# Kernel optimization log

Measured on AMD Instinct MI355X. Metric: run time of the kernel, lower is better.

The kernel has to match this reference:

```python
import jax, jax.numpy as jnp
import numpy as np

N_HEADS = 16
NEG = -1e9  # matches torch masked_fill value


def setup_inputs() -> dict:
    key = jax.random.key(0)
    ks = jax.random.split(key, 8)
    B, S, E = 4, 1024, 1024
    x = jax.random.normal(ks[0], (B, S, E), dtype=jnp.float32)
    event_lengths = jax.random.randint(ks[1], (B,), 1, S + 1)
    scale = 1.0 / np.sqrt(E)
    Wq = jax.random.normal(ks[2], (E, E), dtype=jnp.float32) * scale
    bq = jnp.zeros((E,), dtype=jnp.float32)
    Wk = jax.random.normal(ks[3], (E, E), dtype=jnp.float32) * scale
    bk = jnp.zeros((E,), dtype=jnp.float32)
    Wv = jax.random.normal(ks[4], (E, E), dtype=jnp.float32) * scale
    bv = jnp.zeros((E,), dtype=jnp.float32)
    return {"x": x, "Wq": Wq, "bq": bq, "Wk": Wk, "bk": bk,
            "Wv": Wv, "bv": bv, "event_lengths": event_lengths}


def reference(x, Wq, bq, Wk, bk, Wv, bv, event_lengths):
    B, S, E = x.shape
    H = N_HEADS
    D = E // H
    # fused projections, then split heads: [B,S,E] -> [B,H,S,D]
    def split(t):
        return t.reshape(B, S, H, D).transpose(0, 2, 1, 3)
    q = split(x @ Wq + bq)
    k = split(x @ Wk + bk)
    v = split(x @ Wv + bv)
    scores = jnp.einsum('bhsd,bhtd->bhst', q, k) / jnp.sqrt(jnp.float32(D))
    # rectangular length mask: valid iff row < len AND col < len
    idx = jnp.arange(S)
    valid = idx[None, :] < event_lengths[:, None]           # [B,S]
    mask = valid[:, :, None] & valid[:, None, :]            # [B,S,S]
    scores = jnp.where(mask[:, None, :, :], scores, NEG)
    attn = jax.nn.softmax(scores, axis=-1)
    out = jnp.einsum('bhst,bhtd->bhsd', attn, v)            # [B,H,S,D]
    # concat heads (== torch.cat over head outputs); NOTE: summarize proj is
    # dead code in the original (its result is overwritten), dropout is eval-identity
    return out.transpose(0, 2, 1, 3).reshape(B, S, E)
```

## Files before the change

kernel.cpp:

```cpp
#include <hip/hip_runtime.h>
#include <stdint.h>


using u16     = unsigned short;
using half8   = __attribute__((ext_vector_type(8))) _Float16;
using floatx4 = __attribute__((ext_vector_type(4))) float;

#define MFMA16(a, b, c) __builtin_amdgcn_mfma_f32_16x16x32_f16(a, b, c, 0, 0, 0)

__device__ __forceinline__ u16 f2h(float f) {
  _Float16 h = (_Float16)f; u16 u; __builtin_memcpy(&u, &h, 2); return u;
}

__device__ __forceinline__ void async_cp16(void* lds, const void* g) {
  __builtin_amdgcn_global_load_lds(
      (__attribute__((address_space(1))) uint32_t*)(uintptr_t)g,
      (__attribute__((address_space(3))) uint32_t*)(uint32_t)(uintptr_t)lds,
      16, 0, 0);
}

__global__ void k_prep(const float* __restrict__ x, u16* __restrict__ xh,
                       const float* __restrict__ w0, const float* __restrict__ w1,
                       const float* __restrict__ w2,
                       u16* __restrict__ o0, u16* __restrict__ o1,
                       u16* __restrict__ o2, float* __restrict__ vsum) {
  __shared__ float t[32][33];
  const int bx = blockIdx.x;
  if (bx < 4096) {
    int i = (bx * 256 + threadIdx.x) * 4;
    float4 v = *(const float4*)(x + i);
    ushort4 hv;
    hv.x = f2h(v.x);
    hv.y = f2h(v.y);
    hv.z = f2h(v.z);
    hv.w = f2h(v.w);
    *(ushort4*)(xh + i) = hv;
    if (bx == 0) {
      float4 z = {0.f, 0.f, 0.f, 0.f};
#pragma unroll
      for (int e = 0; e < 4; e++) ((float4*)vsum)[threadIdx.x * 4 + e] = z;
    }
    return;
  }
  const int id = bx - 4096;
  const int z = id >> 10, rem = id & 1023;
  const float* W = z == 0 ? w0 : (z == 1 ? w1 : w2);
  u16* oh = z == 0 ? o0 : (z == 1 ? o1 : o2);
  const int kb = (rem & 31) * 32, nb = (rem >> 5) * 32;
  const int tx = threadIdx.x & 31, ty = threadIdx.x >> 5;
  for (int r = ty; r < 32; r += 8) t[r][tx] = W[(kb + r) * 1024 + nb + tx];
  __syncthreads();
  for (int r = ty; r < 32; r += 8)
    oh[(nb + r) * 1024 + kb + tx] = f2h(t[tx][r]);
}

__launch_bounds__(256, 4)
__global__ void k_proj(const u16* __restrict__ xh,
                       const u16* __restrict__ wqT, const u16* __restrict__ wkT,
                       const u16* __restrict__ wvT,
                       const float* __restrict__ bq, const float* __restrict__ bk,
                       const float* __restrict__ bv,
                       const int* __restrict__ elen,
                       u16* __restrict__ qh, u16* __restrict__ kh,
                       u16* __restrict__ vth, float* __restrict__ vsum) {
  __shared__ u16 Sm[17408];
  const int z = blockIdx.z;
  const int m0 = blockIdx.x * 128, n0 = blockIdx.y * 128;
  if (z != 2 && (m0 & 1023) >= elen[m0 >> 10]) return;

  const u16* wT = z == 0 ? wqT : (z == 1 ? wkT : wvT);
  const float* bias = z == 0 ? bq : (z == 1 ? bk : bv);
  u16* oh = z == 0 ? qh : (z == 1 ? kh : vth);
  const float oscale = (z == 0) ? 0.18033688011112042f : 1.0f;

  const int tid = threadIdx.x, l = tid & 63, w = tid >> 6;
  const int quad = l >> 4, col = l & 15;
  const int wm = (w & 1) * 64, wn = (w >> 1) * 64;

  const int row0 = tid >> 3, ch = tid & 7;
  const int sc8 = (ch ^ (row0 & 7)) * 8;
  int gofs[4], lofs[4];
#pragma unroll
  for (int p = 0; p < 4; p++) {
    gofs[p] = (row0 + 32 * p) * 1024 + sc8;
    lofs[p] = (tid + p * 256) * 8;
  }

  const u16* Ag = xh + m0 * 1024;
  const u16* Bg = wT + n0 * 1024;

  int ar[2][4], br[2][4];
#pragma unroll
  for (int ks = 0; ks < 2; ks++) {
#pragma unroll
    for (int i = 0; i < 4; i++) {
      int r = wm + i * 16 + col;
      ar[ks][i] = r * 64 + (((ks * 4 + quad) ^ (r & 7)) * 8);
    }
#pragma unroll
    for (int j = 0; j < 4; j++) {
      int r = wn + j * 16 + col;
      br[ks][j] = r * 64 + (((ks * 4 + quad) ^ (r & 7)) * 8);
    }
  }

  floatx4 zero4 = {0.f, 0.f, 0.f, 0.f};
  floatx4 acc[4][4];
#pragma unroll
  for (int i = 0; i < 4; i++)
#pragma unroll
    for (int j = 0; j < 4; j++) acc[i][j] = zero4;

  for (int k0 = 0; k0 < 1024; k0 += 64) {
    __syncthreads();
#pragma unroll
    for (int p = 0; p < 4; p++) async_cp16(Sm + lofs[p], Ag + gofs[p] + k0);
#pragma unroll
    for (int p = 0; p < 4; p++)
      async_cp16(Sm + 8192 + lofs[p], Bg + gofs[p] + k0);
    __syncthreads();

#pragma unroll
    for (int ks = 0; ks < 2; ks++) {
      half8 fa[4], fb[4];
#pragma unroll
      for (int i = 0; i < 4; i++) fa[i] = *(const half8*)(Sm + ar[ks][i]);
#pragma unroll
      for (int j = 0; j < 4; j++)
        fb[j] = *(const half8*)(Sm + 8192 + br[ks][j]);
#pragma unroll
      for (int i = 0; i < 4; i++)
#pragma unroll
        for (int j = 0; j < 4; j++) acc[i][j] = MFMA16(fa[i], fb[j], acc[i][j]);
    }
  }

  const int bidx = m0 >> 10;
  const int sbase = m0 & 1023;
  __syncthreads();

#pragma unroll
  for (int j = 0; j < 4; j++) {
    int nloc = wn + j * 16 + col;
    float bb = bias[n0 + nloc];
#pragma unroll
    for (int i = 0; i < 4; i++)
#pragma unroll
      for (int r = 0; r < 4; r++) {
        int mloc = wm + i * 16 + quad * 4 + r;
        Sm[mloc * 136 + nloc] = f2h((acc[i][j][r] + bb) * oscale);
      }
  }
  __syncthreads();

  if (z != 2) {
#pragma unroll
    for (int k = 0; k < 8; k++) {
      int c = tid + k * 256;
      int mloc = c >> 4, n = (c & 15) * 8;
      int hh = (n0 + n) >> 6, d = (n0 + n) & 63;
      half8 vv = *(const half8*)(Sm + mloc * 136 + n);
      *(half8*)(oh + ((bidx * 16 + hh) * 1024 + sbase + mloc) * 64 + d) = vv;
    }
  } else {
#pragma unroll
    for (int k = 0; k < 8; k++) {
      int c = tid + k * 256;
      int nloc = c & 127, s0 = (c >> 7) * 8;
      int hh = (n0 + nloc) >> 6, d = (n0 + nloc) & 63;
      u16 tmp[8];
#pragma unroll
      for (int e = 0; e < 8; e++) tmp[e] = Sm[(s0 + e) * 136 + nloc];
      *(half8*)(vth + ((bidx * 16 + hh) * 64 + d) * 1024 + sbase + s0) =
          *(half8*)tmp;
    }
#pragma unroll
    for (int j = 0; j < 4; j++) {
      int nloc = wn + j * 16 + col;
      float bb = bias[n0 + nloc];
      float part = 16.0f * bb;
#pragma unroll
      for (int i = 0; i < 4; i++)
#pragma unroll
        for (int r = 0; r < 4; r++) part += acc[i][j][r];
      part += __shfl_xor(part, 16, 64);
      part += __shfl_xor(part, 32, 64);
      if (quad == 0) {
        int hh = (n0 + nloc) >> 6, d = (n0 + nloc) & 63;
        unsafeAtomicAdd(vsum + (bidx * 16 + hh) * 64 + d, part);
      }
    }
  }
}

template <int NC>
__device__ __forceinline__ void stageN(u16* lds, const u16* g, int row_stride,
                                       int tid) {
#pragma unroll
  for (int p = 0; p < NC; p++) {
    int slot = (p * 512 + tid) * 8;
    int row = slot >> 6;
    int gp = (slot >> 3) & 7;
    int gl = gp ^ (row & 7);
    async_cp16(lds + slot, g + row * row_stride + gl * 8);
  }
}

__launch_bounds__(512)
__global__ void k_attn(const u16* __restrict__ qh_g,
                       const u16* __restrict__ kh_g,
                       const u16* __restrict__ vth_g,
                       const float* __restrict__ vsum, const int* __restrict__ elen,
                       float* __restrict__ out) {
  __shared__ u16 QP[8192];
  __shared__ u16 Bufs[2][8192];
  const int tid = threadIdx.x, l = tid & 63, w = tid >> 6;
  const int quad = l >> 4, col = l & 15;
  const int tb = w & 3;
  const int qh2 = w >> 2;
  const int id = blockIdx.x;
  const int b = (id + (id >> 8)) & 3;
  const int h = (id >> 2) & 15;
  const int bh = b * 16 + h;
  const int q0 = ((id >> 6) & 7) * 128;
  const int len = elen[b];

  if (q0 >= len) {
    float val = vsum[bh * 64 + l] * (1.0f / 1024.0f);
    float* op = out + (b * 1024 + q0) * 1024 + h * 64 + l;
    for (int r = w; r < 128; r += 8) op[r * 1024] = val;
    return;
  }

  const u16* kh_b  = kh_g + bh * 65536;
  const u16* vth_b = vth_g + bh * 65536;

  stageN<2>(QP, qh_g + (bh * 1024 + q0) * 64, 64, tid);
  stageN<1>(Bufs[0], kh_b, 64, tid);
  stageN<1>(Bufs[0] + 4096, vth_b, 1024, tid);
  __syncthreads();

  half8 qf[4][2];
#pragma unroll
  for (int jj = 0; jj < 4; jj++) {
    int qrow = (qh2 * 4 + jj) * 16 + col;
#pragma unroll
    for (int ks = 0; ks < 2; ks++)
      qf[jj][ks] = *(const half8*)(QP + qrow * 64 +
                                   (((ks * 4 + quad) ^ (qrow & 7)) * 8));
  }
  __syncthreads();

  int ko[2];
#pragma unroll
  for (int ks = 0; ks < 2; ks++) {
    int r = tb * 16 + col;
    ko[ks] = r * 64 + (((ks * 4 + quad) ^ (r & 7)) * 8);
  }
  int po[2];
#pragma unroll
  for (int ks = 0; ks < 2; ks++) {
    int r = w * 16 + col;
    po[ks] = r * 64 + (((ks * 4 + quad) ^ (r & 7)) * 8);
  }
  int kvo[2][4];
#pragma unroll
  for (int ks = 0; ks < 2; ks++)
#pragma unroll
    for (int j = 0; j < 4; j++) {
      int n = j * 16 + col;
      kvo[ks][j] = n * 64 + (((ks * 4 + quad) ^ (n & 7)) * 8);
    }
  int p_wr[4];
  {
    int chv = tb * 2 + (quad >> 1);
#pragma unroll
    for (int jj = 0; jj < 4; jj++) {
      int row = (qh2 * 4 + jj) * 16 + col;
      p_wr[jj] = row * 64 + ((chv ^ (row & 7)) * 8) + (quad & 1) * 4;
    }
  }

  floatx4 zero4 = {0.f, 0.f, 0.f, 0.f};
  floatx4 O[4];
  float lp[4];
#pragma unroll
  for (int j = 0; j < 4; j++) O[j] = zero4;
#pragma unroll
  for (int jj = 0; jj < 4; jj++) lp[jj] = 0.f;

  const int ntt = (len + 63) >> 6;
  for (int tt = 0; tt < ntt; ++tt) {
    const int t0 = tt * 64;
    u16* cur = Bufs[tt & 1];
    if (tt + 1 < ntt) {
      u16* nxt = Bufs[(tt + 1) & 1];
      const int t1 = t0 + 64;
      stageN<1>(nxt, kh_b + t1 * 64, 64, tid);
      stageN<1>(nxt + 4096, vth_b + t1, 1024, tid);
    }

    floatx4 sc[4];
#pragma unroll
    for (int jj = 0; jj < 4; jj++) sc[jj] = zero4;
#pragma unroll
    for (int ks = 0; ks < 2; ks++) {
      half8 kf = *(const half8*)(cur + ko[ks]);
#pragma unroll
      for (int jj = 0; jj < 4; jj++) sc[jj] = MFMA16(kf, qf[jj][ks], sc[jj]);
    }

    if (t0 + 64 > len) {
#pragma unroll
      for (int r = 0; r < 4; r++) {
        bool inv = (t0 + tb * 16 + quad * 4 + r) >= len;
#pragma unroll
        for (int jj = 0; jj < 4; jj++)
          if (inv) sc[jj][r] = -3e38f;
      }
    }

#pragma unroll
    for (int jj = 0; jj < 4; jj++) {
      float e0 = __builtin_exp2f(sc[jj][0]);
      float e1 = __builtin_exp2f(sc[jj][1]);
      float e2 = __builtin_exp2f(sc[jj][2]);
      float e3 = __builtin_exp2f(sc[jj][3]);
      lp[jj] += (e0 + e1) + (e2 + e3);
      uint2 pk;
      pk.x = (uint32_t)f2h(e0) | ((uint32_t)f2h(e1) << 16);
      pk.y = (uint32_t)f2h(e2) | ((uint32_t)f2h(e3) << 16);
      *(uint2*)(QP + p_wr[jj]) = pk;
    }

    asm volatile("s_waitcnt lgkmcnt(0)" ::: "memory");
    __builtin_amdgcn_s_barrier();
    __builtin_amdgcn_sched_barrier(0);

#pragma unroll
    for (int ks = 0; ks < 2; ks++) {
      half8 pa = *(const half8*)(QP + po[ks]);
#pragma unroll
      for (int j = 0; j < 4; j++) {
        half8 vb = *(const half8*)(cur + 4096 + kvo[ks][j]);
        O[j] = MFMA16(pa, vb, O[j]);
      }
    }

    __syncthreads();
  }

  float* lred = (float*)Bufs;
#pragma unroll
  for (int jj = 0; jj < 4; jj++) {
    float v = lp[jj];
    v += __shfl_xor(v, 16, 64);
    v += __shfl_xor(v, 32, 64);
    lp[jj] = v;
  }
  if (quad == 0) {
#pragma unroll
    for (int jj = 0; jj < 4; jj++)
      lred[tb * 128 + (qh2 * 4 + jj) * 16 + col] = lp[jj];
  }
  __syncthreads();

#pragma unroll
  for (int r = 0; r < 4; r++) {
    int qloc = w * 16 + quad * 4 + r;
    int s = q0 + qloc;
    float lr = (lred[qloc] + lred[128 + qloc]) +
               (lred[256 + qloc] + lred[384 + qloc]);
    float invl = 1.0f / lr;
    bool valid = (s < len);
#pragma unroll
    for (int j = 0; j < 4; j++) {
      int d = j * 16 + col;
      float val = valid ? O[j][r] * invl : vsum[bh * 64 + d] * (1.0f / 1024.0f);
      out[(b * 1024 + s) * 1024 + h * 64 + d] = val;
    }
  }
}

extern "C" void kernel_launch(void* const* d_in, const int* in_sizes, int n_in,
                              void* d_out, int out_size, void* d_ws, size_t ws_size,
                              hipStream_t stream) {
  (void)in_sizes; (void)n_in; (void)out_size; (void)ws_size;
  const float* x  = (const float*)d_in[0];
  const float* Wq = (const float*)d_in[1];
  const float* bq = (const float*)d_in[2];
  const float* Wk = (const float*)d_in[3];
  const float* bk = (const float*)d_in[4];
  const float* Wv = (const float*)d_in[5];
  const float* bv = (const float*)d_in[6];
  const int* elen = (const int*)d_in[7];
  float* out = (float*)d_out;

  char* ws = (char*)d_ws;
  const size_t MB = 1024 * 1024;
  u16* xh  = (u16*)(ws + 0 * MB);
  u16* wqT = (u16*)(ws + 8 * MB);
  u16* wkT = (u16*)(ws + 10 * MB);
  u16* wvT = (u16*)(ws + 12 * MB);
  u16* qh  = (u16*)(ws + 14 * MB);
  u16* kh  = (u16*)(ws + 22 * MB);
  u16* vth = (u16*)(ws + 30 * MB);
  float* vsum = (float*)(ws + 38 * MB);

  k_prep<<<7168, 256, 0, stream>>>(x, xh, Wq, Wk, Wv, wqT, wkT, wvT, vsum);
  k_proj<<<dim3(32, 8, 3), 256, 0, stream>>>(xh, wqT, wkT, wvT, bq, bk, bv,
                                             elen, qh, kh, vth, vsum);
  k_attn<<<512, 512, 0, stream>>>(qh, kh, vth, vsum, elen, out);
}
```

Before: 148.7 us.

## Skip V projection tiles past valid length using summed-x GEMV for tail

Result: slower. 164.5 us (+10.6%).

```diff
diff --git a/kernel.cpp b/kernel.cpp
--- a/kernel.cpp
+++ b/kernel.cpp
@@ -10,6 +10,9 @@
 
 __device__ __forceinline__ u16 f2h(float f) {
   _Float16 h = (_Float16)f; u16 u; __builtin_memcpy(&u, &h, 2); return u;
+}
+__device__ __forceinline__ float h2f(u16 u) {
+  _Float16 h; __builtin_memcpy(&h, &u, 2); return (float)h;
 }
 
 __device__ __forceinline__ void async_cp16(void* lds, const void* g) {
@@ -66,16 +69,65 @@
   __shared__ u16 Sm[17408];
   const int z = blockIdx.z;
   const int m0 = blockIdx.x * 128, n0 = blockIdx.y * 128;
-  if (z != 2 && (m0 & 1023) >= elen[m0 >> 10]) return;
+  const int bidx = m0 >> 10;
+  const int sbase = m0 & 1023;
+  const int len = elen[bidx];
+  const int tid = threadIdx.x;
+
+  if (z != 2) {
+    if (sbase >= len) return;
+  } else {
+    const int tstop = ((len + 63) >> 6) << 6;
+    const int vstart = (tstop + 127) & ~127;
+    if (sbase >= vstart) {
+      if (sbase == vstart) {
+        float* xs = (float*)Sm;
+        const int nt = 1024 - vstart;
+        const u16* xb = xh + ((bidx << 10) + vstart) * 1024 + tid * 4;
+        float a0 = 0.f, a1 = 0.f, a2 = 0.f, a3 = 0.f;
+        float b0 = 0.f, b1 = 0.f, b2 = 0.f, b3 = 0.f;
+        int s = 0;
+        for (; s + 2 <= nt; s += 2) {
+          ushort4 h0 = *(const ushort4*)(xb + s * 1024);
+          ushort4 h1 = *(const ushort4*)(xb + s * 1024 + 1024);
+          a0 += h2f(h0.x); a1 += h2f(h0.y); a2 += h2f(h0.z); a3 += h2f(h0.w);
+          b0 += h2f(h1.x); b1 += h2f(h1.y); b2 += h2f(h1.z); b3 += h2f(h1.w);
+        }
+        if (s < nt) {
+          ushort4 h0 = *(const ushort4*)(xb + s * 1024);
+          a0 += h2f(h0.x); a1 += h2f(h0.y); a2 += h2f(h0.z); a3 += h2f(h0.w);
+        }
+        xs[tid * 4 + 0] = a0 + b0;
+        xs[tid * 4 + 1] = a1 + b1;
+        xs[tid * 4 + 2] = a2 + b2;
+        xs[tid * 4 + 3] = a3 + b3;
+        __syncthreads();
+        if (tid < 128) {
+          const int ng = n0 + tid;
+          const u16* wrow = wvT + ng * 1024;
+          float acc = 0.f;
+          for (int k = 0; k < 1024; k += 8) {
+            half8 wv = *(const half8*)(wrow + k);
+#pragma unroll
+            for (int e = 0; e < 8; e++) acc += xs[k + e] * (float)wv[e];
+          }
+          acc += (float)nt * bv[ng];
+          unsafeAtomicAdd(vsum + (bidx << 10) + ng, acc);
+        }
+      }
+      return;
+    }
+  }
 
   const u16* wT = z == 0 ? wqT : (z == 1 ? wkT : wvT);
   const float* bias = z == 0 ? bq : (z == 1 ? bk : bv);
   u16* oh = z == 0 ? qh : (z == 1 ? kh : vth);
   const float oscale = (z == 0) ? 0.18033688011112042f : 1.0f;
 
-  const int tid = threadIdx.x, l = tid & 63, w = tid >> 6;
+  const int l = tid & 63, w = tid >> 6;
   const int quad = l >> 4, col = l & 15;
   const int wm = (w & 1) * 64, wn = (w >> 1) * 64;
+  const bool mlive = (z == 2) || (sbase + wm < len);
 
   const int row0 = tid >> 3, ch = tid & 7;
   const int sc8 = (ch ^ (row0 & 7)) * 8;
@@ -120,23 +172,24 @@
       async_cp16(Sm + 8192 + lofs[p], Bg + gofs[p] + k0);
     __syncthreads();
 
-#pragma unroll
-    for (int ks = 0; ks < 2; ks++) {
-      half8 fa[4], fb[4];
-#pragma unroll
-      for (int i = 0; i < 4; i++) fa[i] = *(const half8*)(Sm + ar[ks][i]);
-#pragma unroll
-      for (int j = 0; j < 4; j++)
-        fb[j] = *(const half8*)(Sm + 8192 + br[ks][j]);
-#pragma unroll
-      for (int i = 0; i < 4; i++)
-#pragma unroll
-        for (int j = 0; j < 4; j++) acc[i][j] = MFMA16(fa[i], fb[j], acc[i][j]);
-    }
-  }
-
-  const int bidx = m0 >> 10;
-  const int sbase = m0 & 1023;
+    if (mlive) {
+#pragma unroll
+      for (int ks = 0; ks < 2; ks++) {
+        half8 fa[4], fb[4];
+#pragma unroll
+        for (int i = 0; i < 4; i++) fa[i] = *(const half8*)(Sm + ar[ks][i]);
+#pragma unroll
+        for (int j = 0; j < 4; j++)
+          fb[j] = *(const half8*)(Sm + 8192 + br[ks][j]);
+#pragma unroll
+        for (int i = 0; i < 4; i++)
+#pragma unroll
+          for (int j = 0; j < 4; j++)
+            acc[i][j] = MFMA16(fa[i], fb[j], acc[i][j]);
+      }
+    }
+  }
+
   __syncthreads();
 
 #pragma unroll
```

## Switch attention to 32x32x16 MFMA with register-resident P via lane shuffles

Applied to the files above, without the earlier changes.

Measured after the change: 151.8 us. +2.1%, slower.

```diff
diff --git a/kernel.cpp b/kernel.cpp
--- a/kernel.cpp
+++ b/kernel.cpp
@@ -5,8 +5,10 @@
 using u16     = unsigned short;
 using half8   = __attribute__((ext_vector_type(8))) _Float16;
 using floatx4 = __attribute__((ext_vector_type(4))) float;
+using f32x16  = __attribute__((ext_vector_type(16))) float;
 
 #define MFMA16(a, b, c) __builtin_amdgcn_mfma_f32_16x16x32_f16(a, b, c, 0, 0, 0)
+#define MFMA32(a, b, c) __builtin_amdgcn_mfma_f32_32x32x16_f16(a, b, c, 0, 0, 0)
 
 __device__ __forceinline__ u16 f2h(float f) {
   _Float16 h = (_Float16)f; u16 u; __builtin_memcpy(&u, &h, 2); return u;
@@ -215,9 +217,9 @@
   __shared__ u16 QP[8192];
   __shared__ u16 Bufs[2][8192];
   const int tid = threadIdx.x, l = tid & 63, w = tid >> 6;
-  const int quad = l >> 4, col = l & 15;
-  const int tb = w & 3;
-  const int qh2 = w >> 2;
+  const int l31 = l & 31, lh = l >> 5;
+  const int qb = w >> 1;
+  const int th = w & 1;
   const int id = blockIdx.x;
   const int b = (id + (id >> 8)) & 3;
   const int h = (id >> 2) & 15;
@@ -240,54 +242,35 @@
   stageN<1>(Bufs[0] + 4096, vth_b, 1024, tid);
   __syncthreads();
 
-  half8 qf[4][2];
-#pragma unroll
-  for (int jj = 0; jj < 4; jj++) {
-    int qrow = (qh2 * 4 + jj) * 16 + col;
-#pragma unroll
-    for (int ks = 0; ks < 2; ks++)
-      qf[jj][ks] = *(const half8*)(QP + qrow * 64 +
-                                   (((ks * 4 + quad) ^ (qrow & 7)) * 8));
-  }
-  __syncthreads();
-
-  int ko[2];
-#pragma unroll
-  for (int ks = 0; ks < 2; ks++) {
-    int r = tb * 16 + col;
-    ko[ks] = r * 64 + (((ks * 4 + quad) ^ (r & 7)) * 8);
-  }
-  int po[2];
-#pragma unroll
-  for (int ks = 0; ks < 2; ks++) {
-    int r = w * 16 + col;
-    po[ks] = r * 64 + (((ks * 4 + quad) ^ (r & 7)) * 8);
-  }
-  int kvo[2][4];
+  half8 qf[4];
+  {
+    int qrow = qb * 32 + l31;
+#pragma unroll
+    for (int kd = 0; kd < 4; kd++)
+      qf[kd] = *(const half8*)(QP + qrow * 64 +
+                               (((kd * 2 + lh) ^ (qrow & 7)) * 8));
+  }
+  int kof[4];
+  {
+    int kr = th * 32 + l31;
+#pragma unroll
+    for (int kd = 0; kd < 4; kd++)
+      kof[kd] = kr * 64 + (((kd * 2 + lh) ^ (kr & 7)) * 8);
+  }
+  int vof[2][2];
 #pragma unroll
   for (int ks = 0; ks < 2; ks++)
 #pragma unroll
-    for (int j = 0; j < 4; j++) {
-      int n = j * 16 + col;
-      kvo[ks][j] = n * 64 + (((ks * 4 + quad) ^ (n & 7)) * 8);
-    }
-  int p_wr[4];
-  {
-    int chv = tb * 2 + (quad >> 1);
-#pragma unroll
-    for (int jj = 0; jj < 4; jj++) {
-      int row = (qh2 * 4 + jj) * 16 + col;
-      p_wr[jj] = row * 64 + ((chv ^ (row & 7)) * 8) + (quad & 1) * 4;
-    }
-  }
-
-  floatx4 zero4 = {0.f, 0.f, 0.f, 0.f};
-  floatx4 O[4];
-  float lp[4];
-#pragma unroll
-  for (int j = 0; j < 4; j++) O[j] = zero4;
-#pragma unroll
-  for (int jj = 0; jj < 4; jj++) lp[jj] = 0.f;
+    for (int db = 0; db < 2; db++) {
+      int vr = db * 32 + l31;
+      int ch = th * 4 + ks * 2 + lh;
+      vof[ks][db] = vr * 64 + ((ch ^ (vr & 7)) * 8);
+    }
+
+  f32x16 O0, O1;
+#pragma unroll
+  for (int r = 0; r < 16; r++) { O0[r] = 0.f; O1[r] = 0.f; }
+  float lsum = 0.f;
 
   const int ntt = (len + 63) >> 6;
   for (int tt = 0; tt < ntt; ++tt) {
@@ -295,89 +278,103 @@
     u16* cur = Bufs[tt & 1];
     if (tt + 1 < ntt) {
       u16* nxt = Bufs[(tt + 1) & 1];
-      const int t1 = t0 + 64;
-      stageN<1>(nxt, kh_b + t1 * 64, 64, tid);
-      stageN<1>(nxt + 4096, vth_b + t1, 1024, tid);
-    }
-
-    floatx4 sc[4];
-#pragma unroll
-    for (int jj = 0; jj < 4; jj++) sc[jj] = zero4;
+      stageN<1>(nxt, kh_b + (t0 + 64) * 64, 64, tid);
+      stageN<1>(nxt + 4096, vth_b + (t0 + 64), 1024, tid);
+    }
+
+    f32x16 sc;
+#pragma unroll
+    for (int r = 0; r < 16; r++) sc[r] = 0.f;
+#pragma unroll
+    for (int kd = 0; kd < 4; kd++) {
+      half8 kf = *(const half8*)(cur + kof[kd]);
+      sc = MFMA32(kf, qf[kd], sc);
+    }
+
+    if (t0 + 64 > len) {
+#pragma unroll
+      for (int r = 0; r < 16; r++) {
+        int t = t0 + th * 32 + (r & 3) + 8 * (r >> 2) + 4 * lh;
+        if (t >= len) sc[r] = -3e38f;
+      }
+    }
+
+    uint32_t pk[8];
+#pragma unroll
+    for (int i = 0; i < 8; i++) {
+      float e0 = __builtin_exp2f(sc[2 * i]);
+      float e1 = __builtin_exp2f(sc[2 * i + 1]);
+      lsum += e0 + e1;
+      pk[i] = (uint32_t)f2h(e0) | ((uint32_t)f2h(e1) << 16);
+    }
+
+    union Frag { uint32_t u[4]; half8 h; };
+    Frag pa[2];
 #pragma unroll
     for (int ks = 0; ks < 2; ks++) {
-      half8 kf = *(const half8*)(cur + ko[ks]);
-#pragma unroll
-      for (int jj = 0; jj < 4; jj++) sc[jj] = MFMA16(kf, qf[jj][ks], sc[jj]);
-    }
-
-    if (t0 + 64 > len) {
-#pragma unroll
-      for (int r = 0; r < 4; r++) {
-        bool inv = (t0 + tb * 16 + quad * 4 + r) >= len;
-#pragma unroll
-        for (int jj = 0; jj < 4; jj++)
-          if (inv) sc[jj][r] = -3e38f;
-      }
-    }
-
-#pragma unroll
-    for (int jj = 0; jj < 4; jj++) {
-      float e0 = __builtin_exp2f(sc[jj][0]);
-      float e1 = __builtin_exp2f(sc[jj][1]);
-      float e2 = __builtin_exp2f(sc[jj][2]);
-      float e3 = __builtin_exp2f(sc[jj][3]);
-      lp[jj] += (e0 + e1) + (e2 + e3);
-      uint2 pk;
-      pk.x = (uint32_t)f2h(e0) | ((uint32_t)f2h(e1) << 16);
-      pk.y = (uint32_t)f2h(e2) | ((uint32_t)f2h(e3) << 16);
-      *(uint2*)(QP + p_wr[jj]) = pk;
-    }
-
-    asm volatile("s_waitcnt lgkmcnt(0)" ::: "memory");
-    __builtin_amdgcn_s_barrier();
-    __builtin_amdgcn_sched_barrier(0);
+      uint32_t p0 = pk[ks * 4 + 0], p1 = pk[ks * 4 + 1];
+      uint32_t p2 = pk[ks * 4 + 2], p3 = pk[ks * 4 + 3];
+      uint32_t x0 = (uint32_t)__shfl_xor((int)p0, 32, 64);
+      uint32_t x1 = (uint32_t)__shfl_xor((int)p1, 32, 64);
+      uint32_t x2 = (uint32_t)__shfl_xor((int)p2, 32, 64);
+      uint32_t x3 = (uint32_t)__shfl_xor((int)p3, 32, 64);
+      pa[ks].u[0] = lh ? x2 : p0;
+      pa[ks].u[1] = lh ? x3 : p1;
+      pa[ks].u[2] = lh ? p2 : x0;
+      pa[ks].u[3] = lh ? p3 : x1;
+    }
 
 #pragma unroll
     for (int ks = 0; ks < 2; ks++) {
-      half8 pa = *(const half8*)(QP + po[ks]);
-#pragma unroll
-      for (int j = 0; j < 4; j++) {
-        half8 vb = *(const half8*)(cur + 4096 + kvo[ks][j]);
-        O[j] = MFMA16(pa, vb, O[j]);
-      }
+      half8 vb0 = *(const half8*)(cur + 4096 + vof[ks][0]);
+      O0 = MFMA32(pa[ks].h, vb0, O0);
+      half8 vb1 = *(const half8*)(cur + 4096 + vof[ks][1]);
+      O1 = MFMA32(pa[ks].h, vb1, O1);
     }
 
     __syncthreads();
   }
 
-  float* lred = (float*)Bufs;
-#pragma unroll
-  for (int jj = 0; jj < 4; jj++) {
-    float v = lp[jj];
-    v += __shfl_xor(v, 16, 64);
-    v += __shfl_xor(v, 32, 64);
-    lp[jj] = v;
-  }
-  if (quad == 0) {
-#pragma unroll
-    for (int jj = 0; jj < 4; jj++)
-      lred[tb * 128 + (qh2 * 4 + jj) * 16 + col] = lp[jj];
+  float lw = lsum + __shfl_xor(lsum, 32, 64);
+  float* lsh = (float*)QP;
+  if (l < 32) lsh[th * 128 + qb * 32 + l] = lw;
+
+  float* osh = (float*)Bufs;
+  if (th) {
+#pragma unroll
+    for (int r = 0; r < 16; r++) {
+      osh[qb * 2048 + r * 64 + l] = O0[r];
+      osh[qb * 2048 + (16 + r) * 64 + l] = O1[r];
+    }
   }
   __syncthreads();
-
-#pragma unroll
-  for (int r = 0; r < 4; r++) {
-    int qloc = w * 16 + quad * 4 + r;
-    int s = q0 + qloc;
-    float lr = (lred[qloc] + lred[128 + qloc]) +
-               (lred[256 + qloc] + lred[384 + qloc]);
-    float invl = 1.0f / lr;
-    bool valid = (s < len);
-#pragma unroll
-    for (int j = 0; j < 4; j++) {
-      int d = j * 16 + col;
-      float val = valid ? O[j][r] * invl : vsum[bh * 64 + d] * (1.0f / 1024.0f);
-      out[(b * 1024 + s) * 1024 + h * 64 + d] = val;
+  if (th) return;
+
+#pragma unroll
+  for (int r = 0; r < 16; r++) {
+    O0[r] += osh[qb * 2048 + r * 64 + l];
+    O1[r] += osh[qb * 2048 + (16 + r) * 64 + l];
+  }
+
+  const float vs0 = vsum[bh * 64 + l31] * (1.0f / 1024.0f);
+  const float vs1 = vsum[bh * 64 + 32 + l31] * (1.0f / 1024.0f);
+#pragma unroll
+  for (int g = 0; g < 4; g++) {
+    int qbase = qb * 32 + 8 * g + 4 * lh;
+    float4 la = *(const float4*)(lsh + qbase);
+    float4 lb = *(const float4*)(lsh + 128 + qbase);
+#pragma unroll
+    for (int i = 0; i < 4; i++) {
+      int s = q0 + qbase + i;
+      float lr = (&la.x)[i] + (&lb.x)[i];
+      float invl = 1.0f / lr;
+      bool valid = (s < len);
+      int r = g * 4 + i;
+      float v0 = valid ? O0[r] * invl : vs0;
+      float v1 = valid ? O1[r] * invl : vs1;
+      float* op = out + (b * 1024 + s) * 1024 + h * 64 + l31;
+      op[0]  = v0;
+      op[32] = v1;
     }
   }
 }
```
